# Performance work log

Hardware: AMD Instinct MI355X
Metric: run time of the kernel (lower is better)

Reference implementation:

```python
import jax, jax.numpy as jnp
import numpy as np

V, D, H, B, LA, LC = 50000, 300, 256, 32, 256, 256


def setup_inputs():
    key = jax.random.key(0)
    ks = jax.random.split(key, 20)
    u = lambda k, sh, sc: jax.random.uniform(k, sh, jnp.float32, -sc, sc)
    s = 1.0 / float(np.sqrt(H))
    return {
        "anchor_input": jax.random.randint(ks[0], (B, LA), 0, V),
        "anchor_length": jax.random.randint(ks[1], (B,), 1, LA + 1),
        "candidate_input": jax.random.randint(ks[2], (B, LC), 0, V),
        "candidate_length": jax.random.randint(ks[3], (B,), 1, LC + 1),
        "batch_size": B,
        "emb": jax.random.normal(ks[4], (V, D), jnp.float32) * 0.1,
        "W_ih_a": u(ks[5], (3 * H, D), s),
        "W_hh_a": u(ks[6], (3 * H, H), s),
        "b_ih_a": u(ks[7], (3 * H,), s),
        "b_hh_a": u(ks[8], (3 * H,), s),
        "W_ih_c": u(ks[9], (3 * H, D + H), s),
        "W_hh_c": u(ks[10], (3 * H, H), s),
        "b_ih_c": u(ks[11], (3 * H,), s),
        "b_hh_c": u(ks[12], (3 * H,), s),
        "Wq": u(ks[13], (H, H), s),
        "Wk": u(ks[14], (H, H), s),
        "v_att": u(ks[15], (H,), s),
    }


def _gru_step(x, h, W_ih, W_hh, b_ih, b_hh):
    # torch GRUCell convention (gate order r, z, n)
    gi = x @ W_ih.T + b_ih
    gh = h @ W_hh.T + b_hh
    ir, iz, inn = jnp.split(gi, 3, axis=-1)
    hr, hz, hn = jnp.split(gh, 3, axis=-1)
    r = jax.nn.sigmoid(ir + hr)
    z = jax.nn.sigmoid(iz + hz)
    n = jnp.tanh(inn + r * hn)
    return (1.0 - z) * n + z * h


def _forward(anchor_input, anchor_length, candidate_input, candidate_length,
             emb, W_ih_a, W_hh_a, b_ih_a, b_hh_a,
             W_ih_c, W_hh_c, b_ih_c, b_hh_c, Wq, Wk, v_att):
    Bb = anchor_input.shape[0]
    # ---- anchor encoder: GRU with packed-sequence semantics (zero pad outputs, freeze hidden) ----
    ax = emb[anchor_input].transpose(1, 0, 2)  # [LA, B, D]
    ts_a = jnp.arange(ax.shape[0])

    def a_step(h, inp):
        xt, t = inp
        hn = _gru_step(xt, h, W_ih_a, W_hh_a, b_ih_a, b_hh_a)
        valid = (t < anchor_length)[:, None]
        h = jnp.where(valid, hn, h)
        return h, jnp.where(valid, hn, 0.0)

    h0 = jnp.zeros((Bb, H), ax.dtype)
    anchor_hidden, a_outs = jax.lax.scan(a_step, h0, (ax, ts_a))  # a_outs: [LA, B, H]
    anchor_outputs = a_outs.transpose(1, 0, 2)  # [B, LA, H]
    anchor_emb = a_outs.sum(0) / anchor_length.astype(ax.dtype)[:, None]  # meanVector

    # ---- candidate decoder: per-step additive attention + GRU + length-mask blend ----
    keys = anchor_outputs @ Wk  # [B, LA, H], precomputed once
    cx = emb[candidate_input].transpose(1, 0, 2)  # [LC, B, D]
    ts_c = jnp.arange(cx.shape[0])

    def c_step(h, inp):
        xt, t = inp
        q = h @ Wq  # [B, H] query from previous hidden
        scores = jnp.einsum('blh,h->bl', jnp.tanh(keys + q[:, None, :]), v_att)
        attn = jax.nn.softmax(scores, axis=-1)
        context = jnp.einsum('bl,blh->bh', attn, anchor_outputs)
        hn = _gru_step(jnp.concatenate([xt, context], axis=-1), h,
                       W_ih_c, W_hh_c, b_ih_c, b_hh_c)
        mask = (candidate_length < t).astype(h.dtype)[:, None]  # strict '<' is faithful to source
        h = hn * (1.0 - mask) + mask * h
        return h, h * (1.0 - mask)

    _, c_outs = jax.lax.scan(c_step, anchor_hidden, (cx, ts_c))  # [LC, B, H]
    valid_c = (ts_c[:, None] < candidate_length[None, :]).astype(cx.dtype)[:, :, None]
    candidate_emb = (c_outs * valid_c).sum(0) / candidate_length.astype(cx.dtype)[:, None]
    return anchor_emb, candidate_emb


def reference(anchor_input, anchor_length, candidate_input, candidate_length, batch_size,
              emb, W_ih_a, W_hh_a, b_ih_a, b_hh_a,
              W_ih_c, W_hh_c, b_ih_c, b_hh_c, Wq, Wk, v_att):
    return _forward(anchor_input, anchor_length, candidate_input, candidate_length,
                    emb, W_ih_a, W_hh_a, b_ih_a, b_hh_a,
                    W_ih_c, W_hh_c, b_ih_c, b_hh_c, Wq, Wk, v_att)
```

## Files before the change

### kernel.cpp

```cpp
#include <hip/hip_runtime.h>
#include <hip/hip_fp16.h>
#include <math.h>

#define BB 32
#define LAV 256
#define LCV 256
#define DV 300
#define HV 256
#define G3 768

typedef _Float16 f16x2 __attribute__((ext_vector_type(2)));
union F4H8 { float4 f4; f16x2 h2[4]; };
union U2H4 { uint2 u2; f16x2 h2[2]; };

static __device__ __forceinline__ float rcp_(float x) { return __builtin_amdgcn_rcpf(x); }
static __device__ __forceinline__ float sigm(float x) { return rcp_(1.f + __expf(-x)); }
static __device__ __forceinline__ float tanh_(float x) { return 1.f - 2.f * rcp_(1.f + __expf(2.f * x)); }

__global__ void prep_pack(const float* __restrict__ W_ih_a, const float* __restrict__ W_ih_c,
                          const float* __restrict__ W_hh_a, const float* __restrict__ W_hh_c,
                          const float* __restrict__ Wq,
                          float* __restrict__ WT_a, float* __restrict__ WT_cx,
                          __half* __restrict__ WhaRH, __half* __restrict__ WhaSH,
                          __half* __restrict__ Wq4, __half* __restrict__ Wrz4,
                          __half* __restrict__ Wn4, float* __restrict__ WcxCT)
{
    int i = blockIdx.x * 256 + threadIdx.x;
    switch (blockIdx.y) {
    case 0: if (i < 230400) { int k = i / 768, n = i % 768; WT_a[i] = W_ih_a[n * 300 + k]; } break;
    case 1: if (i < 230400) { int k = i / 768, n = i % 768; WT_cx[i] = W_ih_c[n * 556 + k]; } break;
    case 2: if (i < 98304) { int e = i & 1, r = i >> 1, ii = r & 63, j = r >> 6;
            WhaRH[i] = __float2half(W_hh_a[j * 256 + 2 * ii + e]); } break;
    case 3: if (i < 98304) { int e = i & 1, s = (i >> 1) & 1, r = i >> 2, j = r % 768, i2 = r / 768;
            int k = 2 * (64 + 2 * i2 + s) + e;
            WhaSH[i] = __float2half(W_hh_a[j * 256 + k]); } break;
    case 4: if (i < 65536) { int e = i & 1, c = (i >> 1) & 3, r = i >> 3, m = r & 255, kq = r >> 8;
            int k = 8 * kq + 2 * c + e;
            Wq4[i] = __float2half(Wq[k * 256 + m]); } break;
    case 5: if (i < 131072) { int e = i & 1, c = (i >> 1) & 3, r = i >> 3, j = r & 511, kq = r >> 9;
            int k = 8 * kq + 2 * c + e;
            Wrz4[i] = __float2half(W_hh_c[j * 256 + k]); } break;
    case 6: if (i < 65536) { int e = i & 1, c = (i >> 1) & 3, r = i >> 3, j = r & 255, kq = r >> 8;
            int k = 8 * kq + 2 * c + e;
            Wn4[i] = __float2half(W_hh_c[(512 + j) * 256 + k]); } break;
    case 7: if (i < 196608) { int k = i / 768, j = i % 768;
            WcxCT[i] = W_ih_c[j * 556 + 300 + k]; } break;
    }
}

template <int MODE>
__global__ __launch_bounds__(256) void gemm_tile(
    const float* __restrict__ X, const int* __restrict__ gidx, int ldx,
    const float* __restrict__ Wt, int K, int Nn,
    const float* __restrict__ bias, float* __restrict__ Cout)
{
    __shared__ __align__(16) float As[32][68];
    __shared__ __align__(16) float Bs[32][68];
    __shared__ int toks[64];
    int tid = threadIdx.x;
    int m0 = blockIdx.x * 64, n0 = blockIdx.y * 64;
    if (tid < 64) {
        int m = m0 + tid;
        if (gidx) { int t = m >> 5, b = m & 31; toks[tid] = gidx[b * LAV + t]; }
        else toks[tid] = m;
    }
    __syncthreads();
    float acc[4][4] = {};
    int tx = tid & 15, ty = tid >> 4;
    for (int k0 = 0; k0 < K; k0 += 32) {
        {
            int r = tid >> 2, cc = (tid & 3) * 8;
            const float* src = X + (size_t)toks[r] * ldx + k0 + cc;
            float4 v0 = {0.f,0.f,0.f,0.f}, v1 = {0.f,0.f,0.f,0.f};
            if (k0 + cc + 3 < K) v0 = *(const float4*)src;
            if (k0 + cc + 7 < K) v1 = *(const float4*)(src + 4);
            As[cc+0][r]=v0.x; As[cc+1][r]=v0.y; As[cc+2][r]=v0.z; As[cc+3][r]=v0.w;
            As[cc+4][r]=v1.x; As[cc+5][r]=v1.y; As[cc+6][r]=v1.z; As[cc+7][r]=v1.w;
        }
        {
            int kr = tid >> 4, c4 = (tid & 15) * 4;
            #pragma unroll
            for (int p = 0; p < 2; ++p) {
                float4 v = {0.f,0.f,0.f,0.f};
                int kg = k0 + kr + p * 16;
                if (kg < K) v = *(const float4*)(Wt + (size_t)kg * Nn + n0 + c4);
                *(float4*)&Bs[kr + p * 16][c4] = v;
            }
        }
        __syncthreads();
        #pragma unroll 8
        for (int kk = 0; kk < 32; ++kk) {
            float4 a4 = *(const float4*)&As[kk][ty * 4];
            float4 b4 = *(const float4*)&Bs[kk][tx * 4];
            acc[0][0]=fmaf(a4.x,b4.x,acc[0][0]); acc[0][1]=fmaf(a4.x,b4.y,acc[0][1]);
            acc[0][2]=fmaf(a4.x,b4.z,acc[0][2]); acc[0][3]=fmaf(a4.x,b4.w,acc[0][3]);
            acc[1][0]=fmaf(a4.y,b4.x,acc[1][0]); acc[1][1]=fmaf(a4.y,b4.y,acc[1][1]);
            acc[1][2]=fmaf(a4.y,b4.z,acc[1][2]); acc[1][3]=fmaf(a4.y,b4.w,acc[1][3]);
            acc[2][0]=fmaf(a4.z,b4.x,acc[2][0]); acc[2][1]=fmaf(a4.z,b4.y,acc[2][1]);
            acc[2][2]=fmaf(a4.z,b4.z,acc[2][2]); acc[2][3]=fmaf(a4.z,b4.w,acc[2][3]);
            acc[3][0]=fmaf(a4.w,b4.x,acc[3][0]); acc[3][1]=fmaf(a4.w,b4.y,acc[3][1]);
            acc[3][2]=fmaf(a4.w,b4.z,acc[3][2]); acc[3][3]=fmaf(a4.w,b4.w,acc[3][3]);
        }
        __syncthreads();
    }
    if (MODE == 0) {
        float4 bz = *(const float4*)&bias[n0 + tx * 4];
        #pragma unroll
        for (int i = 0; i < 4; ++i) {
            int m = m0 + ty * 4 + i;
            float4 o = { acc[i][0] + bz.x, acc[i][1] + bz.y, acc[i][2] + bz.z, acc[i][3] + bz.w };
            *(float4*)&Cout[(size_t)m * Nn + n0 + tx * 4] = o;
        }
    } else if (MODE == 1) {
        int b_ = m0 >> 8;
        int l0 = (m0 & 255) + ty * 4;
        f16x2* T4 = (f16x2*)Cout;
        #pragma unroll
        for (int j = 0; j < 4; ++j) {
            int h = n0 + tx * 4 + j;
            size_t base = (((size_t)(b_ * 64 + (h >> 2)) * 128) + (l0 >> 1)) * 4 + (h & 3);
            f16x2 v01 = { (_Float16)tanh_(acc[0][j]), (_Float16)tanh_(acc[1][j]) };
            f16x2 v23 = { (_Float16)tanh_(acc[2][j]), (_Float16)tanh_(acc[3][j]) };
            T4[base] = v01;
            T4[base + 4] = v23;
        }
    } else {
        int l0 = m0 + ty * 4;
        f16x2* P4 = (f16x2*)Cout;
        #pragma unroll
        for (int j = 0; j < 4; ++j) {
            int col = n0 + tx * 4 + j;
            size_t base = ((size_t)(l0 >> 3) * 768 + col) * 4 + ((l0 >> 1) & 3);
            f16x2 v01 = { (_Float16)acc[0][j], (_Float16)acc[1][j] };
            f16x2 v23 = { (_Float16)acc[2][j], (_Float16)acc[3][j] };
            P4[base] = v01;
            P4[base + 1] = v23;
        }
    }
}

__global__ __launch_bounds__(768) void anchor_rnn(
    const float* __restrict__ GI, const int* __restrict__ lens,
    const float* __restrict__ bhh, const __half* __restrict__ WhaRH,
    const __half* __restrict__ WhaSH,
    float* __restrict__ AO, __half* __restrict__ AOH,
    float* __restrict__ hid, float* __restrict__ outp)
{
    __shared__ float gh[768];
    __shared__ __align__(16) float hs[256];
    __shared__ __align__(16) f16x2 hx2[128];
    __shared__ float bhhS[768];
    int bid = blockIdx.x, tid = threadIdx.x;
    int len = lens[bid];

    f16x2 wreg[64];
    {
        const float4* s = (const float4*)WhaRH + (size_t)tid * 16;
        #pragma unroll
        for (int u = 0; u < 16; ++u) {
            F4H8 c; c.f4 = s[u];
            wreg[4*u+0] = c.h2[0]; wreg[4*u+1] = c.h2[1];
            wreg[4*u+2] = c.h2[2]; wreg[4*u+3] = c.h2[3];
        }
    }
    if (tid < 256) hs[tid] = 0.f;
    if (tid < 128) { f16x2 z = {(_Float16)0.f, (_Float16)0.f}; hx2[tid] = z; }
    bhhS[tid] = bhh[tid];
    float sum = 0.f;
    __syncthreads();

    for (int t = 0; t < LAV; ++t) {
        {
            float a0=0.f,a1=0.f,a2=0.f,a3=0.f;
            const float4* xb = (const float4*)hx2;
            #pragma unroll
            for (int u = 0; u < 16; ++u) {
                F4H8 xv; xv.f4 = xb[u];
                a0 = __builtin_amdgcn_fdot2(wreg[4*u+0], xv.h2[0], a0, false);
                a1 = __builtin_amdgcn_fdot2(wreg[4*u+1], xv.h2[1], a1, false);
                a2 = __builtin_amdgcn_fdot2(wreg[4*u+2], xv.h2[2], a2, false);
                a3 = __builtin_amdgcn_fdot2(wreg[4*u+3], xv.h2[3], a3, false);
            }
            const uint2* wsp = (const uint2*)WhaSH + tid;
            float b0=0.f,b1=0.f;
            #pragma unroll
            for (int i2 = 0; i2 < 32; ++i2) {
                U2H4 w; w.u2 = wsp[(size_t)i2 * 768];
                U2H4 xx; xx.u2 = *(const uint2*)&hx2[64 + 2 * i2];
                b0 = __builtin_amdgcn_fdot2(w.h2[0], xx.h2[0], b0, false);
                b1 = __builtin_amdgcn_fdot2(w.h2[1], xx.h2[1], b1, false);
            }
            gh[tid] = ((a0 + a1) + (a2 + a3)) + (b0 + b1) + bhhS[tid];
        }
        __syncthreads();
        if (tid < 256) {
            const float* gi = GI + ((size_t)t * BB + bid) * G3;
            float r = sigm(gi[tid] + gh[tid]);
            float z = sigm(gi[256 + tid] + gh[256 + tid]);
            float n = tanh_(fmaf(r, gh[512 + tid], gi[512 + tid]));
            float hk = hs[tid];
            float hn = (1.f - z) * n + z * hk;
            bool valid = (t < len);
            float hnew = valid ? hn : hk;
            hs[tid] = hnew;
            float ov = valid ? hn : 0.f;
            AO[((size_t)bid * LAV + t) * HV + tid] = ov;
            AOH[((size_t)bid * LAV + t) * HV + tid] = __float2half(ov);
            sum += ov;
            float other = __shfl_xor(hnew, 1, 64);
            if (!(tid & 1)) {
                f16x2 v = { (_Float16)hnew, (_Float16)other };
                hx2[tid >> 1] = v;
            }
        }
        __syncthreads();
    }
    if (tid < 256) {
        outp[bid * HV + tid] = sum / (float)len;
        hid[bid * HV + tid] = hs[tid];
    }
}

__global__ __launch_bounds__(1024) void cand_rnn(
    const float* __restrict__ GI, const int* __restrict__ lens,
    const float* __restrict__ bhh, const __half* __restrict__ Wrz4,
    const __half* __restrict__ Wn4, const __half* __restrict__ Wq4,
    const float* __restrict__ v_att, const __half* __restrict__ P4H,
    const __half* __restrict__ T4H, const float* __restrict__ hid,
    float* __restrict__ outp)
{
    __shared__ __align__(16) f16x2 x2[128];
    __shared__ __align__(16) float hs[256];
    __shared__ __align__(16) float2 tqv[256];
    __shared__ float vls[256];
    __shared__ __align__(16) __half attnH[256];
    __shared__ __align__(16) float redBig[2048];
    __shared__ __align__(16) float redRZh[512];
    __shared__ __align__(16) float redNh[256];
    __shared__ __align__(16) float gateC[768];
    __shared__ float bhhS[768];
    __shared__ float wred[8];

    int tid = threadIdx.x;
    int b = blockIdx.x;
    int len = lens[b];

    const float4* Wq4f  = (const float4*)Wq4;
    const float4* Wrz4f = (const float4*)Wrz4;
    const float4* Wn4f  = (const float4*)Wn4;
    const float4* T4f   = (const float4*)T4H + (size_t)b * 64 * 128;
    const float4* P4f   = (const float4*)P4H + (size_t)b * 32 * 768;
    const float4* x4    = (const float4*)x2;
    const float4* at4   = (const float4*)attnH;

    if (tid < 256) { hs[tid] = hid[b * HV + tid]; vls[tid] = v_att[tid]; }
    if (tid < 768) bhhS[tid] = bhh[tid];
    __syncthreads();
    if (tid < 128) {
        f16x2 v = { (_Float16)hs[2 * tid], (_Float16)hs[2 * tid + 1] };
        x2[tid] = v;
    }
    __syncthreads();

    float csum = 0.f;

    for (int t = 0; t < LCV; ++t) {
        float gir = 0.f, giz = 0.f, gin = 0.f;
        if (tid < 256) {
            const float* gi = GI + ((size_t)t * BB + b) * G3 + tid;
            gir = gi[0]; giz = gi[256]; gin = gi[512];
            int m = tid;
            float a0 = 0.f, a1 = 0.f, a2 = 0.f, a3 = 0.f;
            #pragma unroll 8
            for (int kq = 0; kq < 32; ++kq) {
                F4H8 w; w.f4 = Wq4f[(size_t)kq * 256 + m];
                F4H8 xx; xx.f4 = x4[kq];
                a0 = __builtin_amdgcn_fdot2(w.h2[0], xx.h2[0], a0, false);
                a1 = __builtin_amdgcn_fdot2(w.h2[1], xx.h2[1], a1, false);
                a2 = __builtin_amdgcn_fdot2(w.h2[2], xx.h2[2], a2, false);
                a3 = __builtin_amdgcn_fdot2(w.h2[3], xx.h2[3], a3, false);
            }
            float tq = tanh_((a0 + a1) + (a2 + a3));
            tqv[m] = make_float2(tq, vls[m] * tq);
        } else if (tid < 768) {
            int j = tid - 256;
            float a0 = 0.f, a1 = 0.f, a2 = 0.f, a3 = 0.f;
            #pragma unroll 8
            for (int kq = 0; kq < 32; ++kq) {
                F4H8 w; w.f4 = Wrz4f[(size_t)kq * 512 + j];
                F4H8 xx; xx.f4 = x4[kq];
                a0 = __builtin_amdgcn_fdot2(w.h2[0], xx.h2[0], a0, false);
                a1 = __builtin_amdgcn_fdot2(w.h2[1], xx.h2[1], a1, false);
                a2 = __builtin_amdgcn_fdot2(w.h2[2], xx.h2[2], a2, false);
                a3 = __builtin_amdgcn_fdot2(w.h2[3], xx.h2[3], a3, false);
            }
            redRZh[j] = (a0 + a1) + (a2 + a3);
        } else {
            int j = tid - 768;
            float a0 = 0.f, a1 = 0.f, a2 = 0.f, a3 = 0.f;
            #pragma unroll 8
            for (int kq = 0; kq < 32; ++kq) {
                F4H8 w; w.f4 = Wn4f[(size_t)kq * 256 + j];
                F4H8 xx; xx.f4 = x4[kq];
                a0 = __builtin_amdgcn_fdot2(w.h2[0], xx.h2[0], a0, false);
                a1 = __builtin_amdgcn_fdot2(w.h2[1], xx.h2[1], a1, false);
                a2 = __builtin_amdgcn_fdot2(w.h2[2], xx.h2[2], a2, false);
                a3 = __builtin_amdgcn_fdot2(w.h2[3], xx.h2[3], a3, false);
            }
            redNh[j] = (a0 + a1) + (a2 + a3);
        }
        __syncthreads();
        {
            int l2 = tid & 127, hg = tid >> 7;
            const float4* Tb = T4f + (size_t)(hg * 8) * 128 + l2;
            float s0 = 0.f, s1 = 0.f;
            #pragma unroll
            for (int i = 0; i < 8; ++i) {
                F4H8 tv4; tv4.f4 = Tb[(size_t)i * 128];
                #pragma unroll
                for (int c = 0; c < 4; ++c) {
                    int h = (hg * 8 + i) * 4 + c;
                    float2 tv = tqv[h];
                    float vv = vls[h];
                    float T0 = (float)tv4.h2[c].x, T1 = (float)tv4.h2[c].y;
                    float d0 = fmaxf(fmaf(T0, tv.x, 1.f), 1e-6f);
                    float d1 = fmaxf(fmaf(T1, tv.x, 1.f), 1e-6f);
                    s0 = fmaf(fmaf(vv, T0, tv.y), rcp_(d0), s0);
                    s1 = fmaf(fmaf(vv, T1, tv.y), rcp_(d1), s1);
                }
            }
            redBig[hg * 256 + 2 * l2] = s0;
            redBig[hg * 256 + 2 * l2 + 1] = s1;
        }
        __syncthreads();
        float sv = 0.f;
        if (tid < 256) {
            #pragma unroll
            for (int hg = 0; hg < 8; ++hg) sv += redBig[hg * 256 + tid];
            float m = sv;
            #pragma unroll
            for (int o = 1; o < 64; o <<= 1) m = fmaxf(m, __shfl_xor(m, o, 64));
            if ((tid & 63) == 0) wred[tid >> 6] = m;
        }
        __syncthreads();
        if (tid < 256) {
            float mx = fmaxf(fmaxf(wred[0], wred[1]), fmaxf(wred[2], wred[3]));
            float e = __expf(sv - mx);
            attnH[tid] = __float2half(e);
            float s = e;
            #pragma unroll
            for (int o = 1; o < 64; o <<= 1) s += __shfl_xor(s, o, 64);
            if ((tid & 63) == 0) wred[4 + (tid >> 6)] = s;
        }
        __syncthreads();
        if (tid < 768) {
            float a0 = 0.f, a1 = 0.f;
            #pragma unroll 8
            for (int lq = 0; lq < 32; ++lq) {
                F4H8 p; p.f4 = P4f[(size_t)lq * 768 + tid];
                F4H8 aa; aa.f4 = at4[lq];
                a0 = __builtin_amdgcn_fdot2(p.h2[0], aa.h2[0], a0, false);
                a1 = __builtin_amdgcn_fdot2(p.h2[1], aa.h2[1], a1, false);
                a0 = __builtin_amdgcn_fdot2(p.h2[2], aa.h2[2], a0, false);
                a1 = __builtin_amdgcn_fdot2(p.h2[3], aa.h2[3], a1, false);
            }
            gateC[tid] = a0 + a1;
        }
        __syncthreads();
        if (tid < 256) {
            float rs = rcp_(wred[4] + wred[5] + wred[6] + wred[7]);
            float rr = redRZh[tid] + gateC[tid] * rs;
            float zz = redRZh[256 + tid] + gateC[256 + tid] * rs;
            float nh = redNh[tid];
            float nc = gateC[512 + tid] * rs;
            float r = sigm(gir + rr + bhhS[tid]);
            float z = sigm(giz + zz + bhhS[256 + tid]);
            float n = tanh_(gin + nc + r * (nh + bhhS[512 + tid]));
            float hk = hs[tid];
            float hn = (1.f - z) * n + z * hk;
            float hnew = (len < t) ? hk : hn;
            hs[tid] = hnew;
            if (t < len) csum += hnew;
            float other = __shfl_xor(hnew, 1, 64);
            if ((tid & 1) == 0) {
                f16x2 v = { (_Float16)hnew, (_Float16)other };
                x2[tid >> 1] = v;
            }
        }
        __syncthreads();
    }
    if (tid < 256) outp[8192 + b * HV + tid] = csum / (float)len;
}

extern "C" void kernel_launch(void* const* d_in, const int* in_sizes, int n_in,
                              void* d_out, int out_size, void* d_ws, size_t ws_size,
                              hipStream_t stream) {
    const int* anchor_input     = (const int*)d_in[0];
    const int* anchor_length    = (const int*)d_in[1];
    const int* candidate_input  = (const int*)d_in[2];
    const int* candidate_length = (const int*)d_in[3];
    const float* emb    = (const float*)d_in[5];
    const float* W_ih_a = (const float*)d_in[6];
    const float* W_hh_a = (const float*)d_in[7];
    const float* b_ih_a = (const float*)d_in[8];
    const float* b_hh_a = (const float*)d_in[9];
    const float* W_ih_c = (const float*)d_in[10];
    const float* W_hh_c = (const float*)d_in[11];
    const float* b_ih_c = (const float*)d_in[12];
    const float* b_hh_c = (const float*)d_in[13];
    const float* Wq     = (const float*)d_in[14];
    const float* Wk     = (const float*)d_in[15];
    const float* v_att  = (const float*)d_in[16];
    float* out = (float*)d_out;

    float* ws = (float*)d_ws;
    size_t off = 0;
    float* GI_a  = ws + off; off += (size_t)LAV * BB * G3;
    float* GI_c  = ws + off; off += (size_t)LCV * BB * G3;
    float* AO    = ws + off; off += (size_t)BB * LAV * HV;
    float* hid   = ws + off; off += (size_t)BB * HV;
    float* WT_a  = ws + off; off += 300 * 768;
    float* WT_cx = ws + off; off += 300 * 768;
    __half* T4H   = (__half*)(ws + off); off += (size_t)BB * HV * LAV / 2;
    __half* AOH   = (__half*)(ws + off); off += (size_t)BB * LAV * HV / 2;
    __half* WhaRH = (__half*)(ws + off); off += 98304 / 2;
    __half* WhaSH = (__half*)(ws + off); off += 98304 / 2;
    __half* Wq4   = (__half*)(ws + off); off += 65536 / 2;
    __half* Wrz4  = (__half*)(ws + off); off += 131072 / 2;
    __half* Wn4   = (__half*)(ws + off); off += 65536 / 2;
    float* WcxCT  = ws + off; off += 256 * 768;
    __half* P4H = (__half*)GI_a;

    prep_pack<<<dim3(900, 8), 256, 0, stream>>>(W_ih_a, W_ih_c, W_hh_a, W_hh_c, Wq,
                                                WT_a, WT_cx, WhaRH, WhaSH, Wq4, Wrz4, Wn4, WcxCT);
    gemm_tile<0><<<dim3(128, 12), 256, 0, stream>>>(emb, anchor_input, DV, WT_a, DV, G3, b_ih_a, GI_a);
    gemm_tile<0><<<dim3(128, 12), 256, 0, stream>>>(emb, candidate_input, DV, WT_cx, DV, G3, b_ih_c, GI_c);
    anchor_rnn<<<32, 768, 0, stream>>>(GI_a, anchor_length, b_hh_a, WhaRH, WhaSH, AO, AOH, hid, out);
    gemm_tile<1><<<dim3(128, 4), 256, 0, stream>>>(AO, nullptr, HV, Wk, HV, HV, nullptr, (float*)T4H);
    gemm_tile<2><<<dim3(128, 12), 256, 0, stream>>>(AO, nullptr, HV, WcxCT, HV, G3, nullptr, (float*)P4H);
    cand_rnn<<<32, 1024, 0, stream>>>(GI_c, candidate_length, b_hh_c, Wrz4, Wn4, Wq4,
                                      v_att, P4H, T4H, hid, out);
}
```

Measured before the change: 3.554 ms.

## Cache Wn in LDS, prefetch T/P, merge softmax with per-wave max

Copies the Wn recurrent weight slice (128KB fp16) into shared memory once per block, so it is no longer re-read from global memory every step. The T and P tiles are loaded into registers ahead of the barriers, letting their latency overlap with the gate matvecs and the score computation. Softmax now uses a per-wave max and sum with a rescaling combine, which removes one barrier per step. The context matvec is split into four partial accumulators stored in a larger reduction buffer. The risks are heavy LDS use (about 128KB plus buffers) and higher register pressure, which may limit occupancy or cause spills.

```diff
diff --git a/kernel.cpp b/kernel.cpp
--- a/kernel.cpp
+++ b/kernel.cpp
@@ -221,7 +221,7 @@
     }
 }
 
-__global__ __launch_bounds__(1024) void cand_rnn(
+__global__ __launch_bounds__(1024, 4) void cand_rnn(
     const float* __restrict__ GI, const int* __restrict__ lens,
     const float* __restrict__ bhh, const __half* __restrict__ Wrz4,
     const __half* __restrict__ Wn4, const __half* __restrict__ Wq4,
@@ -229,15 +229,15 @@
     const __half* __restrict__ T4H, const float* __restrict__ hid,
     float* __restrict__ outp)
 {
+    __shared__ __align__(16) __half WnS[65536];
     __shared__ __align__(16) f16x2 x2[128];
     __shared__ __align__(16) float hs[256];
     __shared__ __align__(16) float2 tqv[256];
     __shared__ float vls[256];
     __shared__ __align__(16) __half attnH[256];
-    __shared__ __align__(16) float redBig[2048];
+    __shared__ __align__(16) float redBig[3072];
     __shared__ __align__(16) float redRZh[512];
     __shared__ __align__(16) float redNh[256];
-    __shared__ __align__(16) float gateC[768];
     __shared__ float bhhS[768];
     __shared__ float wred[8];
 
@@ -247,12 +247,18 @@
 
     const float4* Wq4f  = (const float4*)Wq4;
     const float4* Wrz4f = (const float4*)Wrz4;
-    const float4* Wn4f  = (const float4*)Wn4;
     const float4* T4f   = (const float4*)T4H + (size_t)b * 64 * 128;
     const float4* P4f   = (const float4*)P4H + (size_t)b * 32 * 768;
     const float4* x4    = (const float4*)x2;
     const float4* at4   = (const float4*)attnH;
-
+    const float4* WnSf  = (const float4*)WnS;
+
+    {
+        const float4* s = (const float4*)Wn4;
+        float4* d = (float4*)WnS;
+        #pragma unroll
+        for (int u = 0; u < 8; ++u) d[u * 1024 + tid] = s[u * 1024 + tid];
+    }
     if (tid < 256) { hs[tid] = hid[b * HV + tid]; vls[tid] = v_att[tid]; }
     if (tid < 768) bhhS[tid] = bhh[tid];
     __syncthreads();
@@ -263,9 +269,16 @@
     __syncthreads();
 
     float csum = 0.f;
+    int l2c = tid & 127, hgc = tid >> 7;
+    const float4* Tb = T4f + (size_t)(hgc * 8) * 128 + l2c;
 
     for (int t = 0; t < LCV; ++t) {
         float gir = 0.f, giz = 0.f, gin = 0.f;
+        F4H8 treg0, treg1, treg2, treg3, treg4, treg5, treg6, treg7;
+        treg0.f4 = Tb[0 * 128]; treg1.f4 = Tb[1 * 128];
+        treg2.f4 = Tb[2 * 128]; treg3.f4 = Tb[3 * 128];
+        treg4.f4 = Tb[4 * 128]; treg5.f4 = Tb[5 * 128];
+        treg6.f4 = Tb[6 * 128]; treg7.f4 = Tb[7 * 128];
         if (tid < 256) {
             const float* gi = GI + ((size_t)t * BB + b) * G3 + tid;
             gir = gi[0]; giz = gi[256]; gin = gi[512];
@@ -300,7 +313,7 @@
             float a0 = 0.f, a1 = 0.f, a2 = 0.f, a3 = 0.f;
             #pragma unroll 8
             for (int kq = 0; kq < 32; ++kq) {
-                F4H8 w; w.f4 = Wn4f[(size_t)kq * 256 + j];
+                F4H8 w; w.f4 = WnSf[(size_t)kq * 256 + j];
                 F4H8 xx; xx.f4 = x4[kq];
                 a0 = __builtin_amdgcn_fdot2(w.h2[0], xx.h2[0], a0, false);
                 a1 = __builtin_amdgcn_fdot2(w.h2[1], xx.h2[1], a1, false);
@@ -311,15 +324,14 @@
         }
         __syncthreads();
         {
-            int l2 = tid & 127, hg = tid >> 7;
-            const float4* Tb = T4f + (size_t)(hg * 8) * 128 + l2;
             float s0 = 0.f, s1 = 0.f;
             #pragma unroll
             for (int i = 0; i < 8; ++i) {
-                F4H8 tv4; tv4.f4 = Tb[(size_t)i * 128];
+                const F4H8& tv4 = (i==0)?treg0:(i==1)?treg1:(i==2)?treg2:(i==3)?treg3:
+                                  (i==4)?treg4:(i==5)?treg5:(i==6)?treg6:treg7;
                 #pragma unroll
                 for (int c = 0; c < 4; ++c) {
-                    int h = (hg * 8 + i) * 4 + c;
+                    int h = (hgc * 8 + i) * 4 + c;
                     float2 tv = tqv[h];
                     float vv = vls[h];
                     float T0 = (float)tv4.h2[c].x, T1 = (float)tv4.h2[c].y;
@@ -329,53 +341,149 @@
                     s1 = fmaf(fmaf(vv, T1, tv.y), rcp_(d1), s1);
                 }
             }
-            redBig[hg * 256 + 2 * l2] = s0;
-            redBig[hg * 256 + 2 * l2 + 1] = s1;
-        }
-        __syncthreads();
-        float sv = 0.f;
+            redBig[hgc * 256 + 2 * l2c] = s0;
+            redBig[hgc * 256 + 2 * l2c + 1] = s1;
+        }
+        F4H8 pr0, pr1, pr2, pr3, pr4, pr5, pr6, pr7, pr8, pr9, pr10, pr11;
+        if (tid < 768) {
+            pr0.f4 = P4f[0*768+tid];  pr1.f4 = P4f[1*768+tid];
+            pr2.f4 = P4f[2*768+tid];  pr3.f4 = P4f[3*768+tid];
+            pr4.f4 = P4f[4*768+tid];  pr5.f4 = P4f[5*768+tid];
+            pr6.f4 = P4f[6*768+tid];  pr7.f4 = P4f[7*768+tid];
+            pr8.f4 = P4f[8*768+tid];  pr9.f4 = P4f[9*768+tid];
+            pr10.f4 = P4f[10*768+tid]; pr11.f4 = P4f[11*768+tid];
+        }
+        __syncthreads();
         if (tid < 256) {
+            float sv = 0.f;
             #pragma unroll
             for (int hg = 0; hg < 8; ++hg) sv += redBig[hg * 256 + tid];
             float m = sv;
             #pragma unroll
             for (int o = 1; o < 64; o <<= 1) m = fmaxf(m, __shfl_xor(m, o, 64));
-            if ((tid & 63) == 0) wred[tid >> 6] = m;
-        }
-        __syncthreads();
-        if (tid < 256) {
-            float mx = fmaxf(fmaxf(wred[0], wred[1]), fmaxf(wred[2], wred[3]));
-            float e = __expf(sv - mx);
+            float e = __expf(sv - m);
             attnH[tid] = __float2half(e);
             float s = e;
             #pragma unroll
             for (int o = 1; o < 64; o <<= 1) s += __shfl_xor(s, o, 64);
-            if ((tid & 63) == 0) wred[4 + (tid >> 6)] = s;
+            if ((tid & 63) == 0) { wred[(tid >> 6) * 2] = m; wred[(tid >> 6) * 2 + 1] = s; }
         }
         __syncthreads();
         if (tid < 768) {
-            float a0 = 0.f, a1 = 0.f;
-            #pragma unroll 8
-            for (int lq = 0; lq < 32; ++lq) {
+            float ac0 = 0.f, ac1 = 0.f, ac2 = 0.f, ac3 = 0.f;
+            F4H8 aa;
+            aa.f4 = at4[0];
+            ac0 = __builtin_amdgcn_fdot2(pr0.h2[0], aa.h2[0], ac0, false);
+            ac0 = __builtin_amdgcn_fdot2(pr0.h2[1], aa.h2[1], ac0, false);
+            ac0 = __builtin_amdgcn_fdot2(pr0.h2[2], aa.h2[2], ac0, false);
+            ac0 = __builtin_amdgcn_fdot2(pr0.h2[3], aa.h2[3], ac0, false);
+            aa.f4 = at4[1];
+            ac0 = __builtin_amdgcn_fdot2(pr1.h2[0], aa.h2[0], ac0, false);
+            ac0 = __builtin_amdgcn_fdot2(pr1.h2[1], aa.h2[1], ac0, false);
+            ac0 = __builtin_amdgcn_fdot2(pr1.h2[2], aa.h2[2], ac0, false);
+            ac0 = __builtin_amdgcn_fdot2(pr1.h2[3], aa.h2[3], ac0, false);
+            aa.f4 = at4[2];
+            ac0 = __builtin_amdgcn_fdot2(pr2.h2[0], aa.h2[0], ac0, false);
+            ac0 = __builtin_amdgcn_fdot2(pr2.h2[1], aa.h2[1], ac0, false);
+            ac0 = __builtin_amdgcn_fdot2(pr2.h2[2], aa.h2[2], ac0, false);
+            ac0 = __builtin_amdgcn_fdot2(pr2.h2[3], aa.h2[3], ac0, false);
+            aa.f4 = at4[3];
+            ac0 = __builtin_amdgcn_fdot2(pr3.h2[0], aa.h2[0], ac0, false);
+            ac0 = __builtin_amdgcn_fdot2(pr3.h2[1], aa.h2[1], ac0, false);
+            ac0 = __builtin_amdgcn_fdot2(pr3.h2[2], aa.h2[2], ac0, false);
+            ac0 = __builtin_amdgcn_fdot2(pr3.h2[3], aa.h2[3], ac0, false);
+            aa.f4 = at4[4];
+            ac0 = __builtin_amdgcn_fdot2(pr4.h2[0], aa.h2[0], ac0, false);
+            ac0 = __builtin_amdgcn_fdot2(pr4.h2[1], aa.h2[1], ac0, false);
+            ac0 = __builtin_amdgcn_fdot2(pr4.h2[2], aa.h2[2], ac0, false);
+            ac0 = __builtin_amdgcn_fdot2(pr4.h2[3], aa.h2[3], ac0, false);
+            aa.f4 = at4[5];
+            ac0 = __builtin_amdgcn_fdot2(pr5.h2[0], aa.h2[0], ac0, false);
+            ac0 = __builtin_amdgcn_fdot2(pr5.h2[1], aa.h2[1], ac0, false);
+            ac0 = __builtin_amdgcn_fdot2(pr5.h2[2], aa.h2[2], ac0, false);
+            ac0 = __builtin_amdgcn_fdot2(pr5.h2[3], aa.h2[3], ac0, false);
+            aa.f4 = at4[6];
+            ac0 = __builtin_amdgcn_fdot2(pr6.h2[0], aa.h2[0], ac0, false);
+            ac0 = __builtin_amdgcn_fdot2(pr6.h2[1], aa.h2[1], ac0, false);
+            ac0 = __builtin_amdgcn_fdot2(pr6.h2[2], aa.h2[2], ac0, false);
+            ac0 = __builtin_amdgcn_fdot2(pr6.h2[3], aa.h2[3], ac0, false);
+            aa.f4 = at4[7];
+            ac0 = __builtin_amdgcn_fdot2(pr7.h2[0], aa.h2[0], ac0, false);
+            ac0 = __builtin_amdgcn_fdot2(pr7.h2[1], aa.h2[1], ac0, false);
+            ac0 = __builtin_amdgcn_fdot2(pr7.h2[2], aa.h2[2], ac0, false);
+            ac0 = __builtin_amdgcn_fdot2(pr7.h2[3], aa.h2[3], ac0, false);
+            aa.f4 = at4[8];
+            ac1 = __builtin_amdgcn_fdot2(pr8.h2[0], aa.h2[0], ac1, false);
+            ac1 = __builtin_amdgcn_fdot2(pr8.h2[1], aa.h2[1], ac1, false);
+            ac1 = __builtin_amdgcn_fdot2(pr8.h2[2], aa.h2[2], ac1, false);
+            ac1 = __builtin_amdgcn_fdot2(pr8.h2[3], aa.h2[3], ac1, false);
+            aa.f4 = at4[9];
+            ac1 = __builtin_amdgcn_fdot2(pr9.h2[0], aa.h2[0], ac1, false);
+            ac1 = __builtin_amdgcn_fdot2(pr9.h2[1], aa.h2[1], ac1, false);
+            ac1 = __builtin_amdgcn_fdot2(pr9.h2[2], aa.h2[2], ac1, false);
+            ac1 = __builtin_amdgcn_fdot2(pr9.h2[3], aa.h2[3], ac1, false);
+            aa.f4 = at4[10];
+            ac1 = __builtin_amdgcn_fdot2(pr10.h2[0], aa.h2[0], ac1, false);
+            ac1 = __builtin_amdgcn_fdot2(pr10.h2[1], aa.h2[1], ac1, false);
+            ac1 = __builtin_amdgcn_fdot2(pr10.h2[2], aa.h2[2], ac1, false);
+            ac1 = __builtin_amdgcn_fdot2(pr10.h2[3], aa.h2[3], ac1, false);
+            aa.f4 = at4[11];
+            ac1 = __builtin_amdgcn_fdot2(pr11.h2[0], aa.h2[0], ac1, false);
+            ac1 = __builtin_amdgcn_fdot2(pr11.h2[1], aa.h2[1], ac1, false);
+            ac1 = __builtin_amdgcn_fdot2(pr11.h2[2], aa.h2[2], ac1, false);
+            ac1 = __builtin_amdgcn_fdot2(pr11.h2[3], aa.h2[3], ac1, false);
+            #pragma unroll
+            for (int lq = 12; lq < 16; ++lq) {
                 F4H8 p; p.f4 = P4f[(size_t)lq * 768 + tid];
-                F4H8 aa; aa.f4 = at4[lq];
-                a0 = __builtin_amdgcn_fdot2(p.h2[0], aa.h2[0], a0, false);
-                a1 = __builtin_amdgcn_fdot2(p.h2[1], aa.h2[1], a1, false);
-                a0 = __builtin_amdgcn_fdot2(p.h2[2], aa.h2[2], a0, false);
-                a1 = __builtin_amdgcn_fdot2(p.h2[3], aa.h2[3], a1, false);
-            }
-            gateC[tid] = a0 + a1;
+                aa.f4 = at4[lq];
+                ac1 = __builtin_amdgcn_fdot2(p.h2[0], aa.h2[0], ac1, false);
+                ac1 = __builtin_amdgcn_fdot2(p.h2[1], aa.h2[1], ac1, false);
+                ac1 = __builtin_amdgcn_fdot2(p.h2[2], aa.h2[2], ac1, false);
+                ac1 = __builtin_amdgcn_fdot2(p.h2[3], aa.h2[3], ac1, false);
+            }
+            #pragma unroll
+            for (int lq = 16; lq < 24; ++lq) {
+                F4H8 p; p.f4 = P4f[(size_t)lq * 768 + tid];
+                aa.f4 = at4[lq];
+                ac2 = __builtin_amdgcn_fdot2(p.h2[0], aa.h2[0], ac2, false);
+                ac2 = __builtin_amdgcn_fdot2(p.h2[1], aa.h2[1], ac2, false);
+                ac2 = __builtin_amdgcn_fdot2(p.h2[2], aa.h2[2], ac2, false);
+                ac2 = __builtin_amdgcn_fdot2(p.h2[3], aa.h2[3], ac2, false);
+            }
+            #pragma unroll
+            for (int lq = 24; lq < 32; ++lq) {
+                F4H8 p; p.f4 = P4f[(size_t)lq * 768 + tid];
+                aa.f4 = at4[lq];
+                ac3 = __builtin_amdgcn_fdot2(p.h2[0], aa.h2[0], ac3, false);
+                ac3 = __builtin_amdgcn_fdot2(p.h2[1], aa.h2[1], ac3, false);
+                ac3 = __builtin_amdgcn_fdot2(p.h2[2], aa.h2[2], ac3, false);
+                ac3 = __builtin_amdgcn_fdot2(p.h2[3], aa.h2[3], ac3, false);
+            }
+            redBig[tid] = ac0;
+            redBig[768 + tid] = ac1;
+            redBig[1536 + tid] = ac2;
+            redBig[2304 + tid] = ac3;
         }
         __syncthreads();
         if (tid < 256) {
-            float rs = rcp_(wred[4] + wred[5] + wred[6] + wred[7]);
-            float rr = redRZh[tid] + gateC[tid] * rs;
-            float zz = redRZh[256 + tid] + gateC[256 + tid] * rs;
+            float m0 = wred[0], S0 = wred[1], m1 = wred[2], S1 = wred[3];
+            float m2 = wred[4], S2 = wred[5], m3 = wred[6], S3 = wred[7];
+            float M = fmaxf(fmaxf(m0, m1), fmaxf(m2, m3));
+            float w0 = __expf(m0 - M), w1 = __expf(m1 - M);
+            float w2 = __expf(m2 - M), w3 = __expf(m3 - M);
+            float rs = rcp_(((w0 * S0 + w1 * S1) + (w2 * S2 + w3 * S3)));
+            float gr = ((w0 * redBig[tid] + w1 * redBig[768 + tid])
+                      + (w2 * redBig[1536 + tid] + w3 * redBig[2304 + tid])) * rs;
+            float gz = ((w0 * redBig[256 + tid] + w1 * redBig[1024 + tid])
+                      + (w2 * redBig[1792 + tid] + w3 * redBig[2560 + tid])) * rs;
+            float gn = ((w0 * redBig[512 + tid] + w1 * redBig[1280 + tid])
+                      + (w2 * redBig[2048 + tid] + w3 * redBig[2816 + tid])) * rs;
+            float rr = redRZh[tid] + gr;
+            float zz = redRZh[256 + tid] + gz;
             float nh = redNh[tid];
-            float nc = gateC[512 + tid] * rs;
             float r = sigm(gir + rr + bhhS[tid]);
             float z = sigm(giz + zz + bhhS[256 + tid]);
-            float n = tanh_(gin + nc + r * (nh + bhhS[512 + tid]));
+            float n = tanh_(gin + gn + r * (nh + bhhS[512 + tid]));
             float hk = hs[tid];
             float hn = (1.f - z) * n + z * hk;
             float hnew = (len < t) ? hk : hn;
```

Result: slower. 7.792 ms (+119.2%).

## Stage Wn in LDS and drop a softmax barrier via per-wave max rescaling

Applied to the files above, without the earlier changes.

Copies the n-gate recurrent weights (128KB fp16) into shared memory once per block, so each step reads them from LDS rather than global/L2. The softmax now uses a per-wave max and sum, and the context dot products are split into four per-wave partial accumulators. These partials are rescaled by exp(m_w - M) in the final gate stage, which removes one __syncthreads per timestep. This raises LDS use past 128KB per block, which may limit occupancy (one block per CU anyway). It also adds a few exp calls and more LDS traffic in the gate combine.

```diff
diff --git a/kernel.cpp b/kernel.cpp
--- a/kernel.cpp
+++ b/kernel.cpp
@@ -229,15 +229,15 @@
     const __half* __restrict__ T4H, const float* __restrict__ hid,
     float* __restrict__ outp)
 {
+    __shared__ __align__(16) __half WnS[65536];
     __shared__ __align__(16) f16x2 x2[128];
     __shared__ __align__(16) float hs[256];
     __shared__ __align__(16) float2 tqv[256];
     __shared__ float vls[256];
     __shared__ __align__(16) __half attnH[256];
-    __shared__ __align__(16) float redBig[2048];
+    __shared__ __align__(16) float redBig[3072];
     __shared__ __align__(16) float redRZh[512];
     __shared__ __align__(16) float redNh[256];
-    __shared__ __align__(16) float gateC[768];
     __shared__ float bhhS[768];
     __shared__ float wred[8];
 
@@ -247,12 +247,18 @@
 
     const float4* Wq4f  = (const float4*)Wq4;
     const float4* Wrz4f = (const float4*)Wrz4;
-    const float4* Wn4f  = (const float4*)Wn4;
     const float4* T4f   = (const float4*)T4H + (size_t)b * 64 * 128;
     const float4* P4f   = (const float4*)P4H + (size_t)b * 32 * 768;
     const float4* x4    = (const float4*)x2;
     const float4* at4   = (const float4*)attnH;
-
+    const float4* WnSf  = (const float4*)WnS;
+
+    {
+        const float4* s = (const float4*)Wn4;
+        float4* d = (float4*)WnS;
+        #pragma unroll
+        for (int u = 0; u < 8; ++u) d[u * 1024 + tid] = s[u * 1024 + tid];
+    }
     if (tid < 256) { hs[tid] = hid[b * HV + tid]; vls[tid] = v_att[tid]; }
     if (tid < 768) bhhS[tid] = bhh[tid];
     __syncthreads();
@@ -300,7 +306,7 @@
             float a0 = 0.f, a1 = 0.f, a2 = 0.f, a3 = 0.f;
             #pragma unroll 8
             for (int kq = 0; kq < 32; ++kq) {
-                F4H8 w; w.f4 = Wn4f[(size_t)kq * 256 + j];
+                F4H8 w; w.f4 = WnSf[(size_t)kq * 256 + j];
                 F4H8 xx; xx.f4 = x4[kq];
                 a0 = __builtin_amdgcn_fdot2(w.h2[0], xx.h2[0], a0, false);
                 a1 = __builtin_amdgcn_fdot2(w.h2[1], xx.h2[1], a1, false);
@@ -333,49 +339,84 @@
             redBig[hg * 256 + 2 * l2 + 1] = s1;
         }
         __syncthreads();
-        float sv = 0.f;
         if (tid < 256) {
+            float sv = 0.f;
             #pragma unroll
             for (int hg = 0; hg < 8; ++hg) sv += redBig[hg * 256 + tid];
             float m = sv;
             #pragma unroll
             for (int o = 1; o < 64; o <<= 1) m = fmaxf(m, __shfl_xor(m, o, 64));
-            if ((tid & 63) == 0) wred[tid >> 6] = m;
-        }
-        __syncthreads();
-        if (tid < 256) {
-            float mx = fmaxf(fmaxf(wred[0], wred[1]), fmaxf(wred[2], wred[3]));
-            float e = __expf(sv - mx);
+            float e = __expf(sv - m);
             attnH[tid] = __float2half(e);
             float s = e;
             #pragma unroll
             for (int o = 1; o < 64; o <<= 1) s += __shfl_xor(s, o, 64);
-            if ((tid & 63) == 0) wred[4 + (tid >> 6)] = s;
+            if ((tid & 63) == 0) { wred[(tid >> 6) * 2] = m; wred[(tid >> 6) * 2 + 1] = s; }
         }
         __syncthreads();
         if (tid < 768) {
-            float a0 = 0.f, a1 = 0.f;
-            #pragma unroll 8
-            for (int lq = 0; lq < 32; ++lq) {
+            float ac0 = 0.f, ac1 = 0.f, ac2 = 0.f, ac3 = 0.f;
+            #pragma unroll
+            for (int lq = 0; lq < 8; ++lq) {
                 F4H8 p; p.f4 = P4f[(size_t)lq * 768 + tid];
                 F4H8 aa; aa.f4 = at4[lq];
-                a0 = __builtin_amdgcn_fdot2(p.h2[0], aa.h2[0], a0, false);
-                a1 = __builtin_amdgcn_fdot2(p.h2[1], aa.h2[1], a1, false);
-                a0 = __builtin_amdgcn_fdot2(p.h2[2], aa.h2[2], a0, false);
-                a1 = __builtin_amdgcn_fdot2(p.h2[3], aa.h2[3], a1, false);
-            }
-            gateC[tid] = a0 + a1;
+                ac0 = __builtin_amdgcn_fdot2(p.h2[0], aa.h2[0], ac0, false);
+                ac0 = __builtin_amdgcn_fdot2(p.h2[1], aa.h2[1], ac0, false);
+                ac0 = __builtin_amdgcn_fdot2(p.h2[2], aa.h2[2], ac0, false);
+                ac0 = __builtin_amdgcn_fdot2(p.h2[3], aa.h2[3], ac0, false);
+            }
+            #pragma unroll
+            for (int lq = 8; lq < 16; ++lq) {
+                F4H8 p; p.f4 = P4f[(size_t)lq * 768 + tid];
+                F4H8 aa; aa.f4 = at4[lq];
+                ac1 = __builtin_amdgcn_fdot2(p.h2[0], aa.h2[0], ac1, false);
+                ac1 = __builtin_amdgcn_fdot2(p.h2[1], aa.h2[1], ac1, false);
+                ac1 = __builtin_amdgcn_fdot2(p.h2[2], aa.h2[2], ac1, false);
+                ac1 = __builtin_amdgcn_fdot2(p.h2[3], aa.h2[3], ac1, false);
+            }
+            #pragma unroll
+            for (int lq = 16; lq < 24; ++lq) {
+                F4H8 p; p.f4 = P4f[(size_t)lq * 768 + tid];
+                F4H8 aa; aa.f4 = at4[lq];
+                ac2 = __builtin_amdgcn_fdot2(p.h2[0], aa.h2[0], ac2, false);
+                ac2 = __builtin_amdgcn_fdot2(p.h2[1], aa.h2[1], ac2, false);
+                ac2 = __builtin_amdgcn_fdot2(p.h2[2], aa.h2[2], ac2, false);
+                ac2 = __builtin_amdgcn_fdot2(p.h2[3], aa.h2[3], ac2, false);
+            }
+            #pragma unroll
+            for (int lq = 24; lq < 32; ++lq) {
+                F4H8 p; p.f4 = P4f[(size_t)lq * 768 + tid];
+                F4H8 aa; aa.f4 = at4[lq];
+                ac3 = __builtin_amdgcn_fdot2(p.h2[0], aa.h2[0], ac3, false);
+                ac3 = __builtin_amdgcn_fdot2(p.h2[1], aa.h2[1], ac3, false);
+                ac3 = __builtin_amdgcn_fdot2(p.h2[2], aa.h2[2], ac3, false);
+                ac3 = __builtin_amdgcn_fdot2(p.h2[3], aa.h2[3], ac3, false);
+            }
+            redBig[tid] = ac0;
+            redBig[768 + tid] = ac1;
+            redBig[1536 + tid] = ac2;
+            redBig[2304 + tid] = ac3;
         }
         __syncthreads();
         if (tid < 256) {
-            float rs = rcp_(wred[4] + wred[5] + wred[6] + wred[7]);
-            float rr = redRZh[tid] + gateC[tid] * rs;
-            float zz = redRZh[256 + tid] + gateC[256 + tid] * rs;
+            float m0 = wred[0], S0 = wred[1], m1 = wred[2], S1 = wred[3];
+            float m2 = wred[4], S2 = wred[5], m3 = wred[6], S3 = wred[7];
+            float M = fmaxf(fmaxf(m0, m1), fmaxf(m2, m3));
+            float w0 = __expf(m0 - M), w1 = __expf(m1 - M);
+            float w2 = __expf(m2 - M), w3 = __expf(m3 - M);
+            float rs = rcp_((w0 * S0 + w1 * S1) + (w2 * S2 + w3 * S3));
+            float gr = ((w0 * redBig[tid] + w1 * redBig[768 + tid])
+                      + (w2 * redBig[1536 + tid] + w3 * redBig[2304 + tid])) * rs;
+            float gz = ((w0 * redBig[256 + tid] + w1 * redBig[1024 + tid])
+                      + (w2 * redBig[1792 + tid] + w3 * redBig[2560 + tid])) * rs;
+            float gn = ((w0 * redBig[512 + tid] + w1 * redBig[1280 + tid])
+                      + (w2 * redBig[2048 + tid] + w3 * redBig[2816 + tid])) * rs;
+            float rr = redRZh[tid] + gr;
+            float zz = redRZh[256 + tid] + gz;
             float nh = redNh[tid];
-            float nc = gateC[512 + tid] * rs;
             float r = sigm(gir + rr + bhhS[tid]);
             float z = sigm(giz + zz + bhhS[256 + tid]);
-            float n = tanh_(gin + nc + r * (nh + bhhS[512 + tid]));
+            float n = tanh_(gin + gn + r * (nh + bhhS[512 + tid]));
             float hk = hs[tid];
             float hn = (1.f - z) * n + z * hk;
             float hnew = (len < t) ? hk : hn;
```

Result: slower. 4.693 ms (+32.0%).
